# Performance work log

Hardware: AMD Instinct MI355X
Metric: run time of the kernel (lower is better)

## Reference

```python
import jax, jax.numpy as jnp
import numpy as np

B, S, D, H, F = 2, 2048, 1024, 16, 4096
DH = D // H
EPS = 1e-6


def layer_norm(x, g, b):
    mu = jnp.mean(x, axis=-1, keepdims=True)
    var = jnp.mean(jnp.square(x - mu), axis=-1, keepdims=True)
    return (x - mu) * jax.lax.rsqrt(var + EPS) * g + b


def setup_inputs() -> dict:
    key = jax.random.key(0)
    ks = jax.random.split(key, 12)
    s_in = 1.0 / np.sqrt(D)
    s_ff = 1.0 / np.sqrt(F)
    return {
        "x_enc": jax.random.normal(ks[0], (B, S, D), jnp.float32),
        "x_pos": jax.random.normal(ks[1], (B, S, D), jnp.float32),
        "wq": jax.random.normal(ks[2], (D, D), jnp.float32) * s_in,
        "bq": jnp.zeros((D,), jnp.float32),
        "wk": jax.random.normal(ks[3], (D, D), jnp.float32) * s_in,
        "bk": jnp.zeros((D,), jnp.float32),
        "wv": jax.random.normal(ks[4], (D, D), jnp.float32) * s_in,
        "bv": jnp.zeros((D,), jnp.float32),
        "wc": jax.random.normal(ks[5], (D, D), jnp.float32) * s_in,
        "bc": jnp.zeros((D,), jnp.float32),
        "w1": jax.random.normal(ks[6], (D, F), jnp.float32) * s_in,
        "b1": jnp.zeros((F,), jnp.float32),
        "w2": jax.random.normal(ks[7], (F, D), jnp.float32) * s_ff,
        "b2": jnp.zeros((D,), jnp.float32),
        "g1": jnp.ones((D,), jnp.float32),
        "be1": jnp.zeros((D,), jnp.float32),
        "g2": jnp.ones((D,), jnp.float32),
        "be2": jnp.zeros((D,), jnp.float32),
    }


def reference(x_enc, x_pos, wq, bq, wk, bk, wv, bv, wc, bc, w1, b1, w2, b2, g1, be1, g2, be2):
    x = x_enc + x_pos  # [B,S,D]

    def split_heads(t):  # [B,S,D] -> [B,H,S,DH]
        return t.reshape(B, S, H, DH).transpose(0, 2, 1, 3)

    q = split_heads(x @ wq + bq)
    k = split_heads(x @ wk + bk)
    v = split_heads(x @ wv + bv)

    scale = jax.lax.rsqrt(jnp.asarray(DH, jnp.float32))
    logits = jnp.einsum("bhqd,bhkd->bhqk", q, k) * scale  # [B,H,S,S]
    weights = jax.nn.softmax(logits, axis=-1)
    attn = jnp.einsum("bhqk,bhkd->bhqd", weights, v)  # [B,H,S,DH]
    attn = attn.transpose(0, 2, 1, 3).reshape(B, S, D)
    attn = attn @ wc + bc

    # residual: x + LN(attn_out)   (dropout inactive in eval)
    a = x + layer_norm(attn, g1, be1)
    ffn = jnp.maximum(a @ w1 + b1, 0.0) @ w2 + b2
    out = a + layer_norm(ffn, g2, be2)
    return out
```

## Files before the change

### kernel.cpp

```cpp
#include <hip/hip_runtime.h>
#include <math.h>

#define B_ 2
#define S_ 2048
#define D_ 1024
#define H_ 16
#define F_ 4096

typedef __bf16 bf16_t;
typedef __bf16 bf16x8 __attribute__((ext_vector_type(8)));
typedef __bf16 bf16x4 __attribute__((ext_vector_type(4)));
typedef float f32x4 __attribute__((ext_vector_type(4)));
typedef float f32x16 __attribute__((ext_vector_type(16)));
typedef _Float16 f16x4 __attribute__((ext_vector_type(4)));
typedef _Float16 f16x8 __attribute__((ext_vector_type(8)));
typedef __fp16 h16x2 __attribute__((ext_vector_type(2)));

__device__ __forceinline__ bf16_t f2b(float f) { return (bf16_t)f; }

__device__ __forceinline__ void gld_lds16(const void* g, void* l) {
  __builtin_amdgcn_global_load_lds(
      (const __attribute__((address_space(1))) unsigned int*)g,
      (__attribute__((address_space(3))) unsigned int*)l, 16, 0, 0);
}

__device__ __forceinline__ void transpose_tile(const float* __restrict__ in,
                                               bf16_t* __restrict__ out,
                                               int K, int N, int bx, int by) {
  __shared__ float tile[64][65];
  int k0 = by * 64, n0 = bx * 64;
  int tid = threadIdx.x;
  int col4 = tid & 15;
  int row = tid >> 4;
#pragma unroll
  for (int rr = 0; rr < 4; ++rr) {
    int r = rr * 16 + row;
    float4 v = *reinterpret_cast<const float4*>(in + (size_t)(k0 + r) * N + n0 + col4 * 4);
    tile[r][col4 * 4 + 0] = v.x;
    tile[r][col4 * 4 + 1] = v.y;
    tile[r][col4 * 4 + 2] = v.z;
    tile[r][col4 * 4 + 3] = v.w;
  }
  __syncthreads();
#pragma unroll
  for (int rr = 0; rr < 4; ++rr) {
    int n = rr * 16 + row;
    bf16x4 o;
    o[0] = f2b(tile[col4 * 4 + 0][n]);
    o[1] = f2b(tile[col4 * 4 + 1][n]);
    o[2] = f2b(tile[col4 * 4 + 2][n]);
    o[3] = f2b(tile[col4 * 4 + 3][n]);
    *reinterpret_cast<bf16x4*>(out + (size_t)(n0 + n) * K + k0 + col4 * 4) = o;
  }
}

__global__ __launch_bounds__(256) void prep_kernel(
    const float* __restrict__ xe, const float* __restrict__ xp,
    bf16_t* __restrict__ XB,
    const float* __restrict__ wq, const float* __restrict__ wk,
    const float* __restrict__ wv, const float* __restrict__ wc,
    const float* __restrict__ w1, const float* __restrict__ w2,
    const float* __restrict__ bq, const float* __restrict__ bk,
    const float* __restrict__ bv,
    bf16_t* __restrict__ Wqkvt, bf16_t* __restrict__ wctb,
    bf16_t* __restrict__ w1tb, bf16_t* __restrict__ w2tb,
    float* __restrict__ bqkv) {
  int bid = blockIdx.x;
  if (bid < 4096) {
    int i = bid * 256 + threadIdx.x;
    float4 av = reinterpret_cast<const float4*>(xe)[i];
    float4 bv4 = reinterpret_cast<const float4*>(xp)[i];
    bf16x4 o;
    o[0] = f2b(av.x + bv4.x); o[1] = f2b(av.y + bv4.y);
    o[2] = f2b(av.z + bv4.z); o[3] = f2b(av.w + bv4.w);
    reinterpret_cast<bf16x4*>(XB)[i] = o;
    return;
  }
  int pb = bid - 4096;
  if (pb < 1024) {
    int seg = pb >> 8, local = pb & 255;
    const float* src = seg == 0 ? wq : (seg == 1 ? wk : (seg == 2 ? wv : wc));
    bf16_t* dst = seg == 3 ? wctb : Wqkvt + (size_t)seg * D_ * D_;
    transpose_tile(src, dst, D_, D_, local & 15, local >> 4);
  } else if (pb < 2048) {
    int local = pb - 1024;
    transpose_tile(w1, w1tb, D_, F_, local & 63, local >> 6);
  } else if (pb < 3072) {
    int local = pb - 2048;
    transpose_tile(w2, w2tb, F_, D_, local & 15, local >> 4);
  } else {
    int i = (pb - 3072) * 256 + threadIdx.x;
    const float* src = i < 1024 ? bq : (i < 2048 ? bk : bv);
    bqkv[i] = src[i & 1023];
  }
}


__device__ __forceinline__ void stage_half(const bf16_t* __restrict__ G,
                                           int grow0, int K, int kt,
                                           bf16_t* lb, int tid) {
#pragma unroll
  for (int c = 0; c < 2; ++c) {
    int e = c * 512 + tid;
    int rl = e >> 3, kg = e & 7;
    int kgs = kg ^ (rl & 7);
    gld_lds16(G + (size_t)(grow0 + rl) * K + kt + kgs * 8, lb + e * 8);
  }
}

template <int DBUF, int MH, int SSLOT, int DOWAIT>
__device__ __forceinline__ void gemm_phase4(
    bf16_t* As, bf16_t* Bs, const bf16_t* __restrict__ A,
    const bf16_t* __restrict__ Bt, f32x16 (&acc)[4][2], bf16x8 (&bq)[2][4],
    int bm, int bn, int K, int kt, int tid, int m32, int khalf,
    int ra0, int ra1, int rb) {
  stage_half(A, bm + (SSLOT & 1) * 128, K, kt, As + SSLOT * 8192, tid);
  stage_half(Bt, bn + (SSLOT & 1) * 128, K, kt, Bs + SSLOT * 8192, tid);
  const bf16_t* abase = As + (DBUF * 2 + MH) * 8192;
  const bf16_t* b0 = Bs + (DBUF * 2 + 0) * 8192;
  const bf16_t* b1 = Bs + (DBUF * 2 + 1) * 8192;
  bf16x8 af0[4], af1[4];
#pragma unroll
  for (int kc = 0; kc < 4; ++kc) {
    int kg = ((kc * 2 + khalf) ^ (m32 & 7)) * 8;
    af0[kc] = *reinterpret_cast<const bf16x8*>(abase + ra0 * 64 + kg);
    af1[kc] = *reinterpret_cast<const bf16x8*>(abase + ra1 * 64 + kg);
    if (MH == 0) {
      bq[0][kc] = *reinterpret_cast<const bf16x8*>(b0 + rb * 64 + kg);
      bq[1][kc] = *reinterpret_cast<const bf16x8*>(b1 + rb * 64 + kg);
    }
  }
  __builtin_amdgcn_s_setprio(1);
#pragma unroll
  for (int kc = 0; kc < 4; ++kc) {
    acc[MH * 2 + 0][0] = __builtin_amdgcn_mfma_f32_32x32x16_bf16(
        af0[kc], bq[0][kc], acc[MH * 2 + 0][0], 0, 0, 0);
    acc[MH * 2 + 1][0] = __builtin_amdgcn_mfma_f32_32x32x16_bf16(
        af1[kc], bq[0][kc], acc[MH * 2 + 1][0], 0, 0, 0);
    acc[MH * 2 + 0][1] = __builtin_amdgcn_mfma_f32_32x32x16_bf16(
        af0[kc], bq[1][kc], acc[MH * 2 + 0][1], 0, 0, 0);
    acc[MH * 2 + 1][1] = __builtin_amdgcn_mfma_f32_32x32x16_bf16(
        af1[kc], bq[1][kc], acc[MH * 2 + 1][1], 0, 0, 0);
  }
  __builtin_amdgcn_s_setprio(0);
  if (DOWAIT) asm volatile("s_waitcnt vmcnt(4)" ::: "memory");
  asm volatile("s_waitcnt lgkmcnt(0)" ::: "memory");
  __builtin_amdgcn_s_barrier();
}

__global__ __launch_bounds__(512) void gemm_kernel(
    const bf16_t* __restrict__ A, const bf16_t* __restrict__ Bt,
    const float* __restrict__ bias,
    bf16_t* __restrict__ P0, bf16_t* __restrict__ P1,
    bf16_t* __restrict__ P2, bf16_t* __restrict__ P3,
    _Float16* __restrict__ VTout,
    int M, int N, int K, int relu, int kchunk, int rx, int ry) {
  __shared__ bf16_t As[4 * 8192];
  __shared__ bf16_t Bs[4 * 8192];
  int tid = threadIdx.x;
  int lane = tid & 63, wave = tid >> 6;
  int bx = blockIdx.x, by = blockIdx.y;
  if (rx) {
    int id = by * gridDim.x + bx;
    int j = id & 7, local = id >> 3;
    int regs_x = gridDim.x / rx;
    bx = (j % regs_x) * rx + local % rx;
    by = (j / regs_x) * ry + local / rx;
  }
  int bm = by * 256, bn = bx * 256;
  int wm = wave >> 2, wn = wave & 3;
  int m32 = lane & 31, khalf = lane >> 5;
  int ra0 = wm * 64 + m32, ra1 = ra0 + 32, rb = wn * 32 + m32;
  int z = blockIdx.z;
  int kbeg = z * kchunk;
  int nt = kchunk >> 6, ntm1 = nt - 1;
  f32x16 acc[4][2] = {};

  stage_half(A, bm, K, kbeg, As + 0 * 8192, tid);
  stage_half(Bt, bn, K, kbeg, Bs + 0 * 8192, tid);
  stage_half(A, bm + 128, K, kbeg, As + 1 * 8192, tid);
  stage_half(Bt, bn + 128, K, kbeg, Bs + 1 * 8192, tid);
  stage_half(A, bm, K, kbeg + 64, As + 2 * 8192, tid);
  stage_half(Bt, bn, K, kbeg + 64, Bs + 2 * 8192, tid);
  asm volatile("s_waitcnt vmcnt(4)" ::: "memory");
  __builtin_amdgcn_s_barrier();

  int nt2 = nt >> 1;
  for (int j = 0; j < nt2; ++j) {
    int t1 = 2 * j + 1;
    int t2 = 2 * j + 2 > ntm1 ? ntm1 : 2 * j + 2;
    int t3 = 2 * j + 3 > ntm1 ? ntm1 : 2 * j + 3;
    bf16x8 bq[2][4];
    gemm_phase4<0, 0, 3, 0>(As, Bs, A, Bt, acc, bq, bm, bn, K, kbeg + t1 * 64, tid, m32, khalf, ra0, ra1, rb);
    gemm_phase4<0, 1, 0, 1>(As, Bs, A, Bt, acc, bq, bm, bn, K, kbeg + t2 * 64, tid, m32, khalf, ra0, ra1, rb);
    gemm_phase4<1, 0, 1, 0>(As, Bs, A, Bt, acc, bq, bm, bn, K, kbeg + t2 * 64, tid, m32, khalf, ra0, ra1, rb);
    gemm_phase4<1, 1, 2, 1>(As, Bs, A, Bt, acc, bq, bm, bn, K, kbeg + t3 * 64, tid, m32, khalf, ra0, ra1, rb);
  }

  bf16_t* Cb = z == 0 ? P0 : (z == 1 ? P1 : (z == 2 ? P2 : P3));
#pragma unroll
  for (int ni = 0; ni < 2; ++ni) {
    int n = bn + ni * 128 + wn * 32 + m32;
    float bz = (bias && z == 0) ? bias[n] : 0.f;
#pragma unroll
    for (int mi = 0; mi < 4; ++mi) {
      float vv[16];
#pragma unroll
      for (int r = 0; r < 16; ++r) {
        float v = acc[mi][ni][r] + bz;
        if (relu) v = fmaxf(v, 0.f);
        vv[r] = v;
      }
      int sb = bm + (mi >> 1) * 128 + wm * 64 + (mi & 1) * 32;
      if (VTout && n >= 2048) {
        int h = (n - 2048) >> 6, d = (n - 2048) & 63;
        int bb = sb >> 11;
        _Float16* vtr = VTout + ((size_t)((bb * H_ + h) * 64 + d)) * S_ + (sb & 2047);
#pragma unroll
        for (int g = 0; g < 4; ++g) {
          int off = ((2 * g + khalf) & 3) * 8 + (g >> 1) * 4;
          f16x4 hv;
          hv[0] = (_Float16)vv[g * 4 + 0]; hv[1] = (_Float16)vv[g * 4 + 1];
          hv[2] = (_Float16)vv[g * 4 + 2]; hv[3] = (_Float16)vv[g * 4 + 3];
          *reinterpret_cast<f16x4*>(vtr + off) = hv;
        }
      } else {
#pragma unroll
        for (int r = 0; r < 16; ++r) {
          int m = sb + (r & 3) + 8 * (r >> 2) + 4 * khalf;
          Cb[(size_t)m * N + n] = f2b(vv[r]);
        }
      }
    }
  }
}

__device__ __forceinline__ f16x8 softmax8(f32x4 se, f32x4 so, float kS,
                                          float kB, float& lsum, h16x2 one2) {
  float pe0 = __builtin_amdgcn_exp2f(fmaf(se[0], kS, -kB));
  float pe1 = __builtin_amdgcn_exp2f(fmaf(se[1], kS, -kB));
  float pe2 = __builtin_amdgcn_exp2f(fmaf(se[2], kS, -kB));
  float pe3 = __builtin_amdgcn_exp2f(fmaf(se[3], kS, -kB));
  float po0 = __builtin_amdgcn_exp2f(fmaf(so[0], kS, -kB));
  float po1 = __builtin_amdgcn_exp2f(fmaf(so[1], kS, -kB));
  float po2 = __builtin_amdgcn_exp2f(fmaf(so[2], kS, -kB));
  float po3 = __builtin_amdgcn_exp2f(fmaf(so[3], kS, -kB));
  h16x2 e01 = __builtin_amdgcn_cvt_pkrtz(pe0, pe1);
  h16x2 e23 = __builtin_amdgcn_cvt_pkrtz(pe2, pe3);
  h16x2 q01 = __builtin_amdgcn_cvt_pkrtz(po0, po1);
  h16x2 q23 = __builtin_amdgcn_cvt_pkrtz(po2, po3);
  lsum = __builtin_amdgcn_fdot2(e01, one2, lsum, false);
  lsum = __builtin_amdgcn_fdot2(e23, one2, lsum, false);
  lsum = __builtin_amdgcn_fdot2(q01, one2, lsum, false);
  lsum = __builtin_amdgcn_fdot2(q23, one2, lsum, false);
  union { h16x2 h[4]; f16x8 v; } pu;
  pu.h[0] = e01; pu.h[1] = e23; pu.h[2] = q01; pu.h[3] = q23;
  return pu.v;
}

__global__ __launch_bounds__(512) void attn_kernel(const bf16_t* __restrict__ Q,
                                                   const bf16_t* __restrict__ Kg,
                                                   const _Float16* __restrict__ VT,
                                                   bf16_t* __restrict__ O, int ldq) {
  __shared__ bf16_t Ks[2][128 * 64];
  __shared__ _Float16 Vs[2][64 * 128];
  int pid = blockIdx.x + gridDim.x * (blockIdx.y + gridDim.y * blockIdx.z);
  int nid = (pid & 7) * 32 + (pid >> 3);
  int qt = nid & 7, h = (nid >> 3) & 15, b = nid >> 7;
  int tid = threadIdx.x, wave = tid >> 6, lane = tid & 63;
  int qcol = lane & 15, grp = lane >> 4;
  int qbase = qt * 256 + wave * 32;
  const float kS = 0.125f * 1.4426950408889634f;
  const float kB = 12.0f * 1.4426950408889634f;
  const h16x2 one2 = {(__fp16)1.f, (__fp16)1.f};

  bf16x8 qf[2][2];
#pragma unroll
  for (int qi = 0; qi < 2; ++qi)
#pragma unroll
    for (int c = 0; c < 2; ++c)
      qf[qi][c] = *reinterpret_cast<const bf16x8*>(
          Q + (size_t)(b * S_ + qbase + qi * 16 + qcol) * ldq + h * 64 + c * 32 + grp * 8);
  const _Float16* vtb = VT + (size_t)((b * H_ + h) * 64) * S_;

  f32x4 oacc[2][4] = {};
  float lsum[2] = {0.f, 0.f};

#define ATTN_STAGE(BUF, T0)                                                     \
  {                                                                             \
    _Pragma("unroll") for (int cc = 0; cc < 2; ++cc) {                          \
      int e = cc * 512 + tid;                                                   \
      int row = e >> 3, kg = e & 7, kgs = kg ^ (row & 7);                       \
      gld_lds16(Kg + (size_t)(b * S_ + (T0) + row) * ldq + h * 64 + kgs * 8,    \
                &Ks[BUF][0] + e * 8);                                           \
    }                                                                           \
    _Pragma("unroll") for (int cc = 0; cc < 2; ++cc) {                          \
      int e = cc * 512 + tid;                                                   \
      int d = e >> 4, kc = e & 15, kcs = kc ^ (d & 7);                          \
      gld_lds16(vtb + (size_t)d * S_ + (T0) + kcs * 8, &Vs[BUF][0] + e * 8);    \
    }                                                                           \
  }

  ATTN_STAGE(0, 0);
  __syncthreads();

  int buf = 0;
  for (int t0 = 0; t0 < S_; t0 += 128) {
    if (t0 + 128 < S_) {
      if (buf == 0) ATTN_STAGE(1, t0 + 128) else ATTN_STAGE(0, t0 + 128);
    }
    const bf16_t* ksb = &Ks[buf][0];
    const _Float16* vsb = &Vs[buf][0];
#pragma unroll
    for (int kb2 = 0; kb2 < 4; ++kb2) {
      f32x4 se[2] = {}, so[2] = {};
      int krowe = kb2 * 32 + qcol;
      int krowo = krowe + 16;
#pragma unroll
      for (int c = 0; c < 2; ++c) {
        int gce = (c * 4 + grp) ^ (krowe & 7);
        bf16x8 kfe = *reinterpret_cast<const bf16x8*>(ksb + krowe * 64 + gce * 8);
        int gco = (c * 4 + grp) ^ (krowo & 7);
        bf16x8 kfo = *reinterpret_cast<const bf16x8*>(ksb + krowo * 64 + gco * 8);
#pragma unroll
        for (int qi = 0; qi < 2; ++qi) {
          se[qi] = __builtin_amdgcn_mfma_f32_16x16x32_bf16(kfe, qf[qi][c], se[qi], 0, 0, 0);
          so[qi] = __builtin_amdgcn_mfma_f32_16x16x32_bf16(kfo, qf[qi][c], so[qi], 0, 0, 0);
        }
      }
      f16x8 pf0 = softmax8(se[0], so[0], kS, kB, lsum[0], one2);
      f16x8 pf1 = softmax8(se[1], so[1], kS, kB, lsum[1], one2);
      __builtin_amdgcn_s_setprio(1);
#pragma unroll
      for (int db = 0; db < 4; ++db) {
        int d = db * 16 + qcol;
        int kc = (kb2 * 4 + grp) ^ (d & 7);
        f16x8 vf = *reinterpret_cast<const f16x8*>(vsb + d * 128 + kc * 8);
        oacc[0][db] = __builtin_amdgcn_mfma_f32_16x16x32_f16(vf, pf0, oacc[0][db], 0, 0, 0);
        oacc[1][db] = __builtin_amdgcn_mfma_f32_16x16x32_f16(vf, pf1, oacc[1][db], 0, 0, 0);
      }
      __builtin_amdgcn_s_setprio(0);
    }
    __syncthreads();
    buf ^= 1;
  }
#undef ATTN_STAGE

#pragma unroll
  for (int qi = 0; qi < 2; ++qi) {
    float l = lsum[qi];
    l += __shfl_xor(l, 16, 64);
    l += __shfl_xor(l, 32, 64);
    float inv = 1.f / l;
    size_t rowbase = (size_t)(b * S_ + qbase + qi * 16 + qcol) * D_ + h * 64;
#pragma unroll
    for (int db = 0; db < 4; ++db) {
      bf16x4 ov;
      ov[0] = f2b(oacc[qi][db][0] * inv);
      ov[1] = f2b(oacc[qi][db][1] * inv);
      ov[2] = f2b(oacc[qi][db][2] * inv);
      ov[3] = f2b(oacc[qi][db][3] * inv);
      *reinterpret_cast<bf16x4*>(O + rowbase + db * 16 + grp * 4) = ov;
    }
  }
}

__global__ __launch_bounds__(256) void ln_res_kernel(const bf16_t* Y0,
                                                     const bf16_t* Y1,
                                                     const bf16_t* Y2,
                                                     const bf16_t* Y3,
                                                     int nY,
                                                     const bf16_t* Xres,
                                                     const float* __restrict__ g,
                                                     const float* __restrict__ be,
                                                     float* OutF,
                                                     bf16_t* OutB) {
  int row = blockIdx.x;
  int tid = threadIdx.x, wave = tid >> 6, lane = tid & 63;
  size_t base = (size_t)row * D_;
  bf16x4 y0 = reinterpret_cast<const bf16x4*>(Y0 + base)[tid];
  bf16x4 y1 = reinterpret_cast<const bf16x4*>(Y1 + base)[tid];
  float4 v;
  v.x = (float)y0[0] + (float)y1[0];
  v.y = (float)y0[1] + (float)y1[1];
  v.z = (float)y0[2] + (float)y1[2];
  v.w = (float)y0[3] + (float)y1[3];
  if (nY == 4) {
    bf16x4 y2 = reinterpret_cast<const bf16x4*>(Y2 + base)[tid];
    bf16x4 y3 = reinterpret_cast<const bf16x4*>(Y3 + base)[tid];
    v.x += (float)y2[0] + (float)y3[0];
    v.y += (float)y2[1] + (float)y3[1];
    v.z += (float)y2[2] + (float)y3[2];
    v.w += (float)y2[3] + (float)y3[3];
  }
  float s = v.x + v.y + v.z + v.w;
  float s2 = v.x * v.x + v.y * v.y + v.z * v.z + v.w * v.w;
#pragma unroll
  for (int off = 32; off > 0; off >>= 1) {
    s += __shfl_xor(s, off, 64);
    s2 += __shfl_xor(s2, off, 64);
  }
  __shared__ float red[2][4];
  if (lane == 0) { red[0][wave] = s; red[1][wave] = s2; }
  __syncthreads();
  s = red[0][0] + red[0][1] + red[0][2] + red[0][3];
  s2 = red[1][0] + red[1][1] + red[1][2] + red[1][3];
  float mu = s * (1.f / D_);
  float var = s2 * (1.f / D_) - mu * mu;
  float rstd = rsqrtf(var + 1e-6f);
  bf16x4 xr4 = reinterpret_cast<const bf16x4*>(Xres + base)[tid];
  float4 gv = reinterpret_cast<const float4*>(g)[tid];
  float4 bv = reinterpret_cast<const float4*>(be)[tid];
  float4 o;
  o.x = (float)xr4[0] + (v.x - mu) * rstd * gv.x + bv.x;
  o.y = (float)xr4[1] + (v.y - mu) * rstd * gv.y + bv.y;
  o.z = (float)xr4[2] + (v.z - mu) * rstd * gv.z + bv.z;
  o.w = (float)xr4[3] + (v.w - mu) * rstd * gv.w + bv.w;
  if (OutF) reinterpret_cast<float4*>(OutF + base)[tid] = o;
  if (OutB) {
    bf16x4 ob; ob[0] = f2b(o.x); ob[1] = f2b(o.y); ob[2] = f2b(o.z); ob[3] = f2b(o.w);
    reinterpret_cast<bf16x4*>(OutB + base)[tid] = ob;
  }
}

extern "C" void kernel_launch(void* const* d_in, const int* in_sizes, int n_in,
                              void* d_out, int out_size, void* d_ws, size_t ws_size,
                              hipStream_t stream) {
  const float* x_enc = (const float*)d_in[0];
  const float* x_pos = (const float*)d_in[1];
  const float* wq = (const float*)d_in[2];
  const float* bq = (const float*)d_in[3];
  const float* wk = (const float*)d_in[4];
  const float* bk = (const float*)d_in[5];
  const float* wv = (const float*)d_in[6];
  const float* bv = (const float*)d_in[7];
  const float* wc = (const float*)d_in[8];
  const float* bc = (const float*)d_in[9];
  const float* w1 = (const float*)d_in[10];
  const float* b1 = (const float*)d_in[11];
  const float* w2 = (const float*)d_in[12];
  const float* b2 = (const float*)d_in[13];
  const float* g1 = (const float*)d_in[14];
  const float* be1 = (const float*)d_in[15];
  const float* g2 = (const float*)d_in[16];
  const float* be2 = (const float*)d_in[17];

  const size_t MB = 1024ull * 1024ull;
  char* w = (char*)d_ws;
  bf16_t* F0 = (bf16_t*)(w + 0);
  bf16_t* F1p = (bf16_t*)(w + 8 * MB);
  bf16_t* Wqkvt = (bf16_t*)(w + 32 * MB);
  bf16_t* wctb = (bf16_t*)(w + 38 * MB);
  bf16_t* w1tb = (bf16_t*)(w + 40 * MB);
  bf16_t* w2tb = (bf16_t*)(w + 48 * MB);
  bf16_t* XB = (bf16_t*)(w + 56 * MB);
  bf16_t* QKVB = (bf16_t*)(w + 64 * MB);
  bf16_t* Pp0 = (bf16_t*)(w + 64 * MB);
  bf16_t* Pp1 = (bf16_t*)(w + 72 * MB);
  bf16_t* Pp2 = (bf16_t*)(w + 80 * MB);
  bf16_t* F2 = (bf16_t*)(w + 64 * MB);
  bf16_t* F3 = (bf16_t*)(w + 72 * MB);
  bf16_t* ATTNB = (bf16_t*)(w + 88 * MB);
  float* bqkv = (float*)(w + 96 * MB);
  _Float16* VTg = (_Float16*)(w + 104 * MB);
  bf16_t* Pp3 = (bf16_t*)(w + 104 * MB);
  bf16_t* F1B = (bf16_t*)(w + 112 * MB);

  const int rows = B_ * S_;

  prep_kernel<<<7180, 256, 0, stream>>>(x_enc, x_pos, XB,
                                        wq, wk, wv, wc, w1, w2, bq, bk, bv,
                                        Wqkvt, wctb, w1tb, w2tb, bqkv);

  gemm_kernel<<<dim3(3 * D_ / 256, rows / 256, 1), 512, 0, stream>>>(
      XB, Wqkvt, bqkv, QKVB, nullptr, nullptr, nullptr, VTg,
      rows, 3 * D_, D_, 0, D_, 3, 8);

  attn_kernel<<<dim3(S_ / 256, H_, B_), 512, 0, stream>>>(
      QKVB, QKVB + D_, VTg, ATTNB, 3 * D_);

  gemm_kernel<<<dim3(D_ / 256, rows / 256, 4), 512, 0, stream>>>(
      ATTNB, wctb, bc, Pp0, Pp1, Pp2, Pp3, nullptr,
      rows, D_, D_, 0, D_ / 4, 2, 4);

  ln_res_kernel<<<rows, 256, 0, stream>>>(Pp0, Pp1, Pp2, Pp3, 4, XB, g1, be1,
                                          nullptr, XB);

  gemm_kernel<<<dim3(F_ / 256, rows / 256, 1), 512, 0, stream>>>(
      XB, w1tb, b1, F1B, nullptr, nullptr, nullptr, nullptr,
      rows, F_, D_, 1, D_, 4, 8);

  gemm_kernel<<<dim3(D_ / 256, rows / 256, 4), 512, 0, stream>>>(
      F1B, w2tb, b2, F0, F1p, F2, F3, nullptr,
      rows, D_, F_, 0, F_ / 4, 2, 4);

  ln_res_kernel<<<rows, 256, 0, stream>>>(F0, F1p, F2, F3, 4, XB, g2, be2,
                                          (float*)d_out, nullptr);
}
```

Before: 337.7 us.

## Split GEMM main loop into eight finer phases with per-array staging

Restructures the GEMM software pipeline from four phases per two k-tiles into eight, each issuing one half-tile global-to-LDS load for A or B and running half the k-chunks of MFMAs. The prologue now preloads both B halves of the next tile instead of one A and one B half. Wait counts are adjusted accordingly, and a final vmcnt(0) drains outstanding loads before the epilogue. The aim is finer interleaving of memory traffic with MFMA work, at the cost of twice as many barriers per iteration.

```diff
diff --git a/kernel.cpp b/kernel.cpp
--- a/kernel.cpp
+++ b/kernel.cpp
@@ -108,23 +108,26 @@
   }
 }
 
-template <int DBUF, int MH, int SSLOT, int DOWAIT>
-__device__ __forceinline__ void gemm_phase4(
+template <int BUF, int MH, int KCP, int SARR, int SSLOT, int DOWAIT>
+__device__ __forceinline__ void gemm_phase8(
     bf16_t* As, bf16_t* Bs, const bf16_t* __restrict__ A,
     const bf16_t* __restrict__ Bt, f32x16 (&acc)[4][2], bf16x8 (&bq)[2][4],
     int bm, int bn, int K, int kt, int tid, int m32, int khalf,
     int ra0, int ra1, int rb) {
-  stage_half(A, bm + (SSLOT & 1) * 128, K, kt, As + SSLOT * 8192, tid);
-  stage_half(Bt, bn + (SSLOT & 1) * 128, K, kt, Bs + SSLOT * 8192, tid);
-  const bf16_t* abase = As + (DBUF * 2 + MH) * 8192;
-  const bf16_t* b0 = Bs + (DBUF * 2 + 0) * 8192;
-  const bf16_t* b1 = Bs + (DBUF * 2 + 1) * 8192;
-  bf16x8 af0[4], af1[4];
-#pragma unroll
-  for (int kc = 0; kc < 4; ++kc) {
+  if (SARR == 0)
+    stage_half(A, bm + (SSLOT & 1) * 128, K, kt, As + SSLOT * 8192, tid);
+  else
+    stage_half(Bt, bn + (SSLOT & 1) * 128, K, kt, Bs + SSLOT * 8192, tid);
+  const bf16_t* abase = As + (BUF * 2 + MH) * 8192;
+  const bf16_t* b0 = Bs + (BUF * 2 + 0) * 8192;
+  const bf16_t* b1 = Bs + (BUF * 2 + 1) * 8192;
+  bf16x8 af0[2], af1[2];
+#pragma unroll
+  for (int k2 = 0; k2 < 2; ++k2) {
+    int kc = KCP * 2 + k2;
     int kg = ((kc * 2 + khalf) ^ (m32 & 7)) * 8;
-    af0[kc] = *reinterpret_cast<const bf16x8*>(abase + ra0 * 64 + kg);
-    af1[kc] = *reinterpret_cast<const bf16x8*>(abase + ra1 * 64 + kg);
+    af0[k2] = *reinterpret_cast<const bf16x8*>(abase + ra0 * 64 + kg);
+    af1[k2] = *reinterpret_cast<const bf16x8*>(abase + ra1 * 64 + kg);
     if (MH == 0) {
       bq[0][kc] = *reinterpret_cast<const bf16x8*>(b0 + rb * 64 + kg);
       bq[1][kc] = *reinterpret_cast<const bf16x8*>(b1 + rb * 64 + kg);
@@ -132,18 +135,19 @@
   }
   __builtin_amdgcn_s_setprio(1);
 #pragma unroll
-  for (int kc = 0; kc < 4; ++kc) {
+  for (int k2 = 0; k2 < 2; ++k2) {
+    int kc = KCP * 2 + k2;
     acc[MH * 2 + 0][0] = __builtin_amdgcn_mfma_f32_32x32x16_bf16(
-        af0[kc], bq[0][kc], acc[MH * 2 + 0][0], 0, 0, 0);
+        af0[k2], bq[0][kc], acc[MH * 2 + 0][0], 0, 0, 0);
     acc[MH * 2 + 1][0] = __builtin_amdgcn_mfma_f32_32x32x16_bf16(
-        af1[kc], bq[0][kc], acc[MH * 2 + 1][0], 0, 0, 0);
+        af1[k2], bq[0][kc], acc[MH * 2 + 1][0], 0, 0, 0);
     acc[MH * 2 + 0][1] = __builtin_amdgcn_mfma_f32_32x32x16_bf16(
-        af0[kc], bq[1][kc], acc[MH * 2 + 0][1], 0, 0, 0);
+        af0[k2], bq[1][kc], acc[MH * 2 + 0][1], 0, 0, 0);
     acc[MH * 2 + 1][1] = __builtin_amdgcn_mfma_f32_32x32x16_bf16(
-        af1[kc], bq[1][kc], acc[MH * 2 + 1][1], 0, 0, 0);
+        af1[k2], bq[1][kc], acc[MH * 2 + 1][1], 0, 0, 0);
   }
   __builtin_amdgcn_s_setprio(0);
-  if (DOWAIT) asm volatile("s_waitcnt vmcnt(4)" ::: "memory");
+  if (DOWAIT) asm volatile("s_waitcnt vmcnt(6)" ::: "memory");
   asm volatile("s_waitcnt lgkmcnt(0)" ::: "memory");
   __builtin_amdgcn_s_barrier();
 }
@@ -180,22 +184,28 @@
   stage_half(Bt, bn, K, kbeg, Bs + 0 * 8192, tid);
   stage_half(A, bm + 128, K, kbeg, As + 1 * 8192, tid);
   stage_half(Bt, bn + 128, K, kbeg, Bs + 1 * 8192, tid);
-  stage_half(A, bm, K, kbeg + 64, As + 2 * 8192, tid);
   stage_half(Bt, bn, K, kbeg + 64, Bs + 2 * 8192, tid);
+  stage_half(Bt, bn + 128, K, kbeg + 64, Bs + 3 * 8192, tid);
   asm volatile("s_waitcnt vmcnt(4)" ::: "memory");
   __builtin_amdgcn_s_barrier();
 
   int nt2 = nt >> 1;
   for (int j = 0; j < nt2; ++j) {
-    int t1 = 2 * j + 1;
+    int kt1 = kbeg + (2 * j + 1) * 64;
     int t2 = 2 * j + 2 > ntm1 ? ntm1 : 2 * j + 2;
     int t3 = 2 * j + 3 > ntm1 ? ntm1 : 2 * j + 3;
+    int kt2 = kbeg + t2 * 64, kt3 = kbeg + t3 * 64;
     bf16x8 bq[2][4];
-    gemm_phase4<0, 0, 3, 0>(As, Bs, A, Bt, acc, bq, bm, bn, K, kbeg + t1 * 64, tid, m32, khalf, ra0, ra1, rb);
-    gemm_phase4<0, 1, 0, 1>(As, Bs, A, Bt, acc, bq, bm, bn, K, kbeg + t2 * 64, tid, m32, khalf, ra0, ra1, rb);
-    gemm_phase4<1, 0, 1, 0>(As, Bs, A, Bt, acc, bq, bm, bn, K, kbeg + t2 * 64, tid, m32, khalf, ra0, ra1, rb);
-    gemm_phase4<1, 1, 2, 1>(As, Bs, A, Bt, acc, bq, bm, bn, K, kbeg + t3 * 64, tid, m32, khalf, ra0, ra1, rb);
-  }
+    gemm_phase8<0, 0, 0, 0, 2, 0>(As, Bs, A, Bt, acc, bq, bm, bn, K, kt1, tid, m32, khalf, ra0, ra1, rb);
+    gemm_phase8<0, 0, 1, 0, 3, 1>(As, Bs, A, Bt, acc, bq, bm, bn, K, kt1, tid, m32, khalf, ra0, ra1, rb);
+    gemm_phase8<0, 1, 0, 1, 0, 0>(As, Bs, A, Bt, acc, bq, bm, bn, K, kt2, tid, m32, khalf, ra0, ra1, rb);
+    gemm_phase8<0, 1, 1, 1, 1, 1>(As, Bs, A, Bt, acc, bq, bm, bn, K, kt2, tid, m32, khalf, ra0, ra1, rb);
+    gemm_phase8<1, 0, 0, 0, 0, 0>(As, Bs, A, Bt, acc, bq, bm, bn, K, kt2, tid, m32, khalf, ra0, ra1, rb);
+    gemm_phase8<1, 0, 1, 0, 1, 1>(As, Bs, A, Bt, acc, bq, bm, bn, K, kt2, tid, m32, khalf, ra0, ra1, rb);
+    gemm_phase8<1, 1, 0, 1, 2, 0>(As, Bs, A, Bt, acc, bq, bm, bn, K, kt3, tid, m32, khalf, ra0, ra1, rb);
+    gemm_phase8<1, 1, 1, 1, 3, 1>(As, Bs, A, Bt, acc, bq, bm, bn, K, kt3, tid, m32, khalf, ra0, ra1, rb);
+  }
+  asm volatile("s_waitcnt vmcnt(0)" ::: "memory");
 
   bf16_t* Cb = z == 0 ? P0 : (z == 1 ? P1 : (z == 2 ? P2 : P3));
 #pragma unroll
```

After: 350.0 us. +3.6%, slower.
